# Kernel tuning notes

Measured on AMD Instinct MI355X. Metric: run time of the kernel, lower is better.

The kernel has to match this reference:

```python
import jax, jax.numpy as jnp
import numpy as np
import math

E = 16          # num_experts
TOP_K = 2       # num_experts_per_tok (used as capacity_factor in EC routing)
D = 1024        # embed_dim
F = 4096        # expert_hidden_dim = mlp_ratio * D
SH = 2048       # shared intermediate = F * n_shared_experts // mlp_ratio


def setup_inputs() -> dict:
    key = jax.random.key(0)
    ks = jax.random.split(key, 10)
    s = lambda k, shape, fan: jax.random.normal(k, shape, jnp.float32) / np.sqrt(fan)
    return {
        "x": jax.random.normal(ks[0], (32, 256, D), jnp.float32),
        "gate_w": s(ks[1], (E, D), D),                 # ECMoEGate.weight
        "up_w": s(ks[2], (E, F, D), D),                # fused_up.weight
        "up_b": s(ks[3], (E, F), D),                   # fused_up.bias
        "gw": s(ks[4], (E, F, D), D),                  # fused_gate.weight
        "gb": s(ks[5], (E, F), D),                     # fused_gate.bias
        "down_w": s(ks[6], (E, D, F), F),              # fused_down.weight
        "down_b": s(ks[7], (E, D), F),                 # fused_down.bias
        "sh_gate_w": s(ks[8], (SH, D), D),             # shared_experts.gate_proj
        "sh_up_w": s(ks[9], (SH, D), D),               # shared_experts.up_proj
        "sh_down_w": s(jax.random.fold_in(key, 11), (D, SH), SH),  # shared_experts.down_proj
    }


def reference(x, gate_w, up_w, up_b, gw, gb, down_w, down_b, sh_gate_w, sh_up_w, sh_down_w):
    B, S, Dm = x.shape
    h = x.reshape(-1, Dm)                               # [T, D]
    T = h.shape[0]
    # gate: sigmoid scores, expert-choice top-k over tokens per expert
    scores = jax.nn.sigmoid(h @ gate_w.T)               # [T, E]
    cap = math.ceil(T / E * TOP_K)                      # capacity per expert
    topk_score, topk_ids = jax.lax.top_k(scores.T, cap) # [E, cap]
    # dispatch: gather tokens per expert
    xin = h[topk_ids]                                   # [E, cap, D]
    # batched expert GLU (baddbmm equivalent)
    up = jnp.einsum('ecd,efd->ecf', xin, up_w) + up_b[:, None, :]
    g = jnp.einsum('ecd,efd->ecf', xin, gw) + gb[:, None, :]
    eo = jax.nn.silu(g) * up                            # [E, cap, F]
    eo = jnp.einsum('ecf,edf->ecd', eo, down_w) + down_b[:, None, :]
    # combine: weighted scatter-add back to token positions
    flat = (eo * topk_score[..., None]).reshape(-1, Dm) # [E*cap, D]
    out = jnp.zeros_like(h).at[topk_ids.reshape(-1)].add(flat)
    out = out.reshape(B, S, Dm)
    # shared dense GLU MLP (SiLU)
    shared = (jax.nn.silu(jnp.einsum('bsd,fd->bsf', x, sh_gate_w))
              * jnp.einsum('bsd,fd->bsf', x, sh_up_w))
    shared = jnp.einsum('bsf,df->bsd', shared, sh_down_w)
    return out + shared
```

## Files before the change

kernel.cpp:

```cpp
#include <hip/hip_runtime.h>
#include <hip/hip_bf16.h>

#define Tn 8192
#define Dn 1024
#define Fn 4096
#define SHn 2048
#define En 16
#define CAPn 1024

typedef __bf16 bf16_t;
typedef bf16_t bf16x8 __attribute__((ext_vector_type(8)));
typedef float f32x4 __attribute__((ext_vector_type(4)));

__device__ __forceinline__ unsigned short f2bf(float f) {
  unsigned int u = __builtin_bit_cast(unsigned int, f);
  u += 0x7FFFu + ((u >> 16) & 1u);
  return (unsigned short)(u >> 16);
}
__device__ __forceinline__ unsigned int pack2(float a, float b) {
  return (unsigned int)f2bf(a) | ((unsigned int)f2bf(b) << 16);
}

__device__ __forceinline__ void gload16(const void* g, void* l) {
  __builtin_amdgcn_global_load_lds(
      (const __attribute__((address_space(1))) unsigned int*)g,
      (__attribute__((address_space(3))) unsigned int*)l, 16, 0, 0);
}

__global__ __launch_bounds__(256) void kcvt(const float* __restrict__ s,
                                            unsigned short* __restrict__ d, int n8) {
  int i = blockIdx.x * 256 + threadIdx.x;
  int stride = gridDim.x * 256;
  const float4* sv = (const float4*)s;
  for (; i < n8; i += stride) {
    float4 a = sv[2 * i], b = sv[2 * i + 1];
    uint4 u = { pack2(a.x, a.y), pack2(a.z, a.w), pack2(b.x, b.y), pack2(b.z, b.w) };
    ((uint4*)d)[i] = u;
  }
}

__global__ __launch_bounds__(256) void kscores(const float* __restrict__ x,
                                               const float* __restrict__ gw,
                                               float* __restrict__ sc) {
  __shared__ float sx[Dn];
  int tid = threadIdx.x, tok = blockIdx.x;
  ((float4*)sx)[tid] = ((const float4*)(x + (size_t)tok * Dn))[tid];
  __syncthreads();
  int e = tid >> 4, kl = tid & 15;
  const float4* w = (const float4*)(gw + e * Dn);
  const float4* xv = (const float4*)sx;
  float acc = 0.f;
#pragma unroll
  for (int j = 0; j < 16; ++j) {
    float4 a = w[kl + 16 * j], b = xv[kl + 16 * j];
    acc += a.x * b.x + a.y * b.y + a.z * b.z + a.w * b.w;
  }
#pragma unroll
  for (int off = 8; off; off >>= 1) acc += __shfl_xor(acc, off, 64);
  if (kl == 0) sc[(size_t)e * Tn + tok] = 1.f / (1.f + expf(-acc));
}

__global__ __launch_bounds__(256) void kselect(const float* __restrict__ scores,
                                               int* __restrict__ ids,
                                               float* __restrict__ oscore) {
  __shared__ unsigned int keys[Tn];
  __shared__ unsigned int hist[256];
  __shared__ unsigned int sh_prefix, sh_k, sh_cnt, sh_eq;
  __shared__ int eqlist[1024];
  const int tid = threadIdx.x, e = blockIdx.x;
  const float* row = scores + (size_t)e * Tn;
  for (int i = 0; i < Tn / 256; ++i)
    keys[tid + i * 256] = __float_as_uint(row[tid + i * 256]);
  if (tid == 0) { sh_prefix = 0u; sh_k = CAPn; }
  __syncthreads();
  for (int shift = 24; shift >= 0; shift -= 8) {
    hist[tid] = 0u;
    __syncthreads();
    unsigned int prefix = sh_prefix;
    unsigned int mask = (shift == 24) ? 0u : (0xFFFFFFFFu << (shift + 8));
    for (int i = 0; i < Tn / 256; ++i) {
      unsigned int kk = keys[tid + i * 256];
      if ((kk & mask) == prefix) atomicAdd(&hist[(kk >> shift) & 255], 1u);
    }
    __syncthreads();
    if (tid == 0) {
      unsigned int k = sh_k, c = 0; int b;
      for (b = 255; b >= 0; --b) { c += hist[b]; if (c >= k) break; }
      sh_k = k - (c - hist[b]);
      sh_prefix = prefix | ((unsigned int)b << shift);
    }
    __syncthreads();
  }
  const unsigned int thr = sh_prefix;
  if (tid == 0) { sh_cnt = 0u; sh_eq = 0u; }
  __syncthreads();
  const int base = e * CAPn;
  for (int i = 0; i < Tn / 256; ++i) {
    int t = tid + i * 256;
    unsigned int kk = keys[t];
    if (kk > thr) {
      unsigned int p = atomicAdd(&sh_cnt, 1u);
      ids[base + p] = t;
      oscore[base + p] = __uint_as_float(kk);
    } else if (kk == thr) {
      unsigned int p = atomicAdd(&sh_eq, 1u);
      if (p < 1024u) eqlist[p] = t;
    }
  }
  __syncthreads();
  if (tid == 0) {
    int need = CAPn - (int)sh_cnt;
    int m = (int)sh_eq; if (m > 1024) m = 1024;
    for (int j = 0; j < need; ++j) {
      int best = 1 << 30, bi = 0;
      for (int i2 = 0; i2 < m; ++i2)
        if (eqlist[i2] < best) { best = eqlist[i2]; bi = i2; }
      eqlist[bi] = 1 << 30;
      ids[base + (int)sh_cnt + j] = best;
      oscore[base + (int)sh_cnt + j] = __uint_as_float(thr);
    }
  }
}

template <int BN, int NOPS, bool GATHER, int EPI>
__global__ __launch_bounds__(512, 2) void kgemm8(
    const unsigned short* __restrict__ Ab, const int* __restrict__ idsg,
    const unsigned short* __restrict__ B1b, const unsigned short* __restrict__ B2b,
    const float* __restrict__ bias1, const float* __restrict__ bias2,
    const float* __restrict__ scg, void* __restrict__ OutV,
    int N, int Mz, int K, int MBc, int NBc) {
  constexpr int BM = 256;
  constexpr int NF = (BN / 4) / 16;
  constexpr int BRPW = BN / 8;
  constexpr int BISS = BRPW / 8;
  constexpr unsigned A_OFF = 0;
  constexpr unsigned B1_OFF = 32768;
  constexpr unsigned B2_OFF = 32768u + (unsigned)BN * 128u;

  __shared__ alignas(16) unsigned char lds[2][65536];
  __shared__ int sIds[BM];
  __shared__ float sSc[BM];

  const int tid = threadIdx.x;
  const int lane = tid & 63, w = tid >> 6;
  const int wm = w >> 2, wn = w & 3;
  const int lrow = lane & 15, lk = lane >> 4;
  const int lr = lane >> 3, lc = lane & 7;
  const int srcb = ((lc ^ lr) << 4);

  const int nwg = gridDim.x;
  const int cpx = nwg >> 3;
  const int bid = blockIdx.x;
  const int swz = (bid & 7) * cpx + (bid >> 3);
  const int bm = swz % MBc;
  const int bn = (swz / MBc) % NBc;
  const int z  = swz / (NBc * MBc);
  const int row0 = bm * BM;

  if (tid < BM) {
    if (GATHER || EPI == 2) {
      sIds[tid] = idsg[z * CAPn + row0 + tid];
      if (EPI == 2) sSc[tid] = scg[z * CAPn + row0 + tid];
    }
  }
  __syncthreads();

  const size_t ks = (size_t)K * 2;
  const unsigned char* Az = (const unsigned char*)Ab + (EPI == 2 ? (size_t)z * Mz * ks : 0);
  const unsigned char* B1z = (const unsigned char*)B1b + (size_t)z * N * ks;
  const unsigned char* B2z = (NOPS == 2) ? (const unsigned char*)B2b + (size_t)z * N * ks : nullptr;

  const unsigned char* aS[4];
#pragma unroll
  for (int i = 0; i < 4; ++i) {
    int rr = w * 32 + 8 * i + lr;
    size_t arow = GATHER ? (size_t)sIds[rr] : (size_t)(row0 + rr);
    aS[i] = Az + arow * ks + srcb;
  }
  const unsigned char* b1S[BISS];
  const unsigned char* b2S[BISS];
#pragma unroll
  for (int i = 0; i < BISS; ++i) {
    int rr = bn * BN + w * BRPW + 8 * i + lr;
    b1S[i] = B1z + (size_t)rr * ks + srcb;
    if (NOPS == 2) b2S[i] = B2z + (size_t)rr * ks + srcb;
  }

  auto STG = [&](int idx, unsigned char* buf, int kb) {
    if (idx < 4) {
      gload16(aS[idx] + kb, buf + A_OFF + (unsigned)(w * 32 + 8 * idx) * 128u);
    } else if (NOPS == 2) {
      if (idx < 6)
        gload16(b1S[idx - 4] + kb, buf + B1_OFF + (unsigned)(w * BRPW + 8 * (idx - 4)) * 128u);
      else
        gload16(b2S[idx - 6] + kb, buf + B2_OFF + (unsigned)(w * BRPW + 8 * (idx - 6)) * 128u);
    } else {
      gload16(b1S[idx - 4] + kb, buf + B1_OFF + (unsigned)(w * BRPW + 8 * (idx - 4)) * 128u);
    }
  };

  f32x4 acc[NOPS][8][NF];
#pragma unroll
  for (int o = 0; o < NOPS; ++o)
#pragma unroll
    for (int m = 0; m < 8; ++m)
#pragma unroll
      for (int n = 0; n < NF; ++n) acc[o][m][n] = {0.f, 0.f, 0.f, 0.f};

#pragma unroll
  for (int i = 0; i < 8; ++i) STG(i, lds[0], 0);

  const int NT = K >> 6;
  int c = 0;
  for (int t = 0; t < NT; ++t) {
    unsigned char* bufc = lds[c];
    unsigned char* bufn = lds[c ^ 1];
    if (t + 1 < NT) {
      const int kb = (t + 1) * 128;
#pragma unroll
      for (int i = 0; i < 8; ++i) STG(i, bufn, kb);
      asm volatile("s_waitcnt vmcnt(8)" ::: "memory");
    } else {
      asm volatile("s_waitcnt vmcnt(0)" ::: "memory");
    }
    __builtin_amdgcn_s_barrier();
    __builtin_amdgcn_sched_barrier(0);

    bf16x8 bv[NOPS][NF][2];
#pragma unroll
    for (int n = 0; n < NF; ++n)
#pragma unroll
      for (int kk = 0; kk < 2; ++kk) {
        unsigned off = (unsigned)(wn * (BN / 4) + n * 16 + lrow) * 128u +
                       ((unsigned)((kk * 4 + lk) ^ (lrow & 7)) << 4);
        bv[0][n][kk] = *(const bf16x8*)(bufc + B1_OFF + off);
        if (NOPS == 2) bv[1][n][kk] = *(const bf16x8*)(bufc + B2_OFF + off);
      }
#pragma unroll
    for (int p = 0; p < 4; ++p) {
      bf16x8 av[2][2];
#pragma unroll
      for (int mm = 0; mm < 2; ++mm)
#pragma unroll
        for (int kk = 0; kk < 2; ++kk) {
          unsigned off = (unsigned)(wm * 128 + p * 32 + mm * 16 + lrow) * 128u +
                         ((unsigned)((kk * 4 + lk) ^ (lrow & 7)) << 4);
          av[mm][kk] = *(const bf16x8*)(bufc + A_OFF + off);
        }
      __builtin_amdgcn_s_setprio(1);
#pragma unroll
      for (int mm = 0; mm < 2; ++mm)
#pragma unroll
        for (int n = 0; n < NF; ++n)
#pragma unroll
          for (int kk = 0; kk < 2; ++kk) {
            acc[0][2 * p + mm][n] = __builtin_amdgcn_mfma_f32_16x16x32_bf16(
                av[mm][kk], bv[0][n][kk], acc[0][2 * p + mm][n], 0, 0, 0);
            if (NOPS == 2)
              acc[1][2 * p + mm][n] = __builtin_amdgcn_mfma_f32_16x16x32_bf16(
                  av[mm][kk], bv[1][n][kk], acc[1][2 * p + mm][n], 0, 0, 0);
          }
      __builtin_amdgcn_s_setprio(0);
    }
    __builtin_amdgcn_sched_barrier(0);
    __builtin_amdgcn_s_barrier();
    c ^= 1;
  }

  if (EPI == 0) {
    unsigned short* H = (unsigned short*)OutV;
#pragma unroll
    for (int n = 0; n < NF; ++n) {
      int col = bn * BN + wn * (BN / 4) + n * 16 + lrow;
      float bg = bias1 ? bias1[(size_t)z * N + col] : 0.f;
      float bu = bias2 ? bias2[(size_t)z * N + col] : 0.f;
#pragma unroll
      for (int mq = 0; mq < 8; ++mq) {
#pragma unroll
        for (int j = 0; j < 4; ++j) {
          float g = acc[0][mq][n][j] + bg;
          float u = (NOPS == 2 ? acc[1][mq][n][j] : 0.f) + bu;
          float h = g / (1.f + __expf(-g)) * u;
          int row = row0 + wm * 128 + mq * 16 + lk * 4 + j;
          H[(size_t)z * Mz * N + (size_t)row * N + col] = f2bf(h);
        }
      }
    }
  } else {
    float* Out = (float*)OutV;
#pragma unroll
    for (int n = 0; n < NF; ++n) {
      int col = bn * BN + wn * (BN / 4) + n * 16 + lrow;
      float bb = bias1 ? bias1[(size_t)z * N + col] : 0.f;
#pragma unroll
      for (int mq = 0; mq < 8; ++mq) {
#pragma unroll
        for (int j = 0; j < 4; ++j) {
          int rl = wm * 128 + mq * 16 + lk * 4 + j;
          float v = acc[0][mq][n][j] + bb;
          if (EPI == 2) {
            atomicAdd(Out + (size_t)sIds[rl] * Dn + col, sSc[rl] * v);
          } else {
            Out[(size_t)(row0 + rl) * Dn + col] = v;
          }
        }
      }
    }
  }
}

extern "C" void kernel_launch(void* const* d_in, const int* in_sizes, int n_in,
                              void* d_out, int out_size, void* d_ws, size_t ws_size,
                              hipStream_t stream) {
  const float* x      = (const float*)d_in[0];
  const float* gate_w = (const float*)d_in[1];
  const float* up_w   = (const float*)d_in[2];
  const float* up_b   = (const float*)d_in[3];
  const float* gw     = (const float*)d_in[4];
  const float* gb     = (const float*)d_in[5];
  const float* down_w = (const float*)d_in[6];
  const float* down_b = (const float*)d_in[7];
  const float* shg    = (const float*)d_in[8];
  const float* shu    = (const float*)d_in[9];
  const float* shd    = (const float*)d_in[10];
  float* out = (float*)d_out;

  const size_t H_BYTES  = (size_t)En * CAPn * Fn * 2;
  const size_t XB_BYTES = (size_t)Tn * Dn * 2;
  const size_t WE_BYTES = (size_t)En * Fn * Dn * 2;
  const size_t SH_BYTES = (size_t)SHn * Dn * 2;
  const size_t SC_BYTES = (size_t)En * Tn * 4;
  const size_t ID_BYTES = (size_t)En * CAPn * 4;
  const size_t need = H_BYTES + XB_BYTES + 3 * WE_BYTES + 3 * SH_BYTES +
                      SC_BYTES + 2 * ID_BYTES;
  if (ws_size < need) return;

  char* p = (char*)d_ws;
  unsigned short* H    = (unsigned short*)p; p += H_BYTES;
  unsigned short* xb   = (unsigned short*)p; p += XB_BYTES;
  unsigned short* upb  = (unsigned short*)p; p += WE_BYTES;
  unsigned short* gwb  = (unsigned short*)p; p += WE_BYTES;
  unsigned short* dwb  = (unsigned short*)p; p += WE_BYTES;
  unsigned short* shgb = (unsigned short*)p; p += SH_BYTES;
  unsigned short* shub = (unsigned short*)p; p += SH_BYTES;
  unsigned short* shdb = (unsigned short*)p; p += SH_BYTES;
  float* scores = (float*)p; p += SC_BYTES;
  int* ids      = (int*)p;  p += ID_BYTES;
  float* osc    = (float*)p;

  kcvt<<<2048, 256, 0, stream>>>(x, xb, Tn * Dn / 8);
  kscores<<<Tn, 256, 0, stream>>>(x, gate_w, scores);
  kselect<<<En, 256, 0, stream>>>(scores, ids, osc);
  kcvt<<<2048, 256, 0, stream>>>(up_w, upb, En * Fn * Dn / 8);
  kcvt<<<2048, 256, 0, stream>>>(gw, gwb, En * Fn * Dn / 8);
  kcvt<<<2048, 256, 0, stream>>>(down_w, dwb, En * Dn * Fn / 8);
  kcvt<<<256, 256, 0, stream>>>(shg, shgb, SHn * Dn / 8);
  kcvt<<<256, 256, 0, stream>>>(shu, shub, SHn * Dn / 8);
  kcvt<<<256, 256, 0, stream>>>(shd, shdb, Dn * SHn / 8);

  kgemm8<128, 2, false, 0><<<(Tn / 256) * (SHn / 128), 512, 0, stream>>>(
      xb, nullptr, shgb, shub, nullptr, nullptr, nullptr, H,
      SHn, Tn, Dn, Tn / 256, SHn / 128);
  kgemm8<256, 1, false, 1><<<(Tn / 256) * (Dn / 256), 512, 0, stream>>>(
      H, nullptr, shdb, nullptr, nullptr, nullptr, nullptr, out,
      Dn, Tn, SHn, Tn / 256, Dn / 256);
  kgemm8<128, 2, true, 0><<<(CAPn / 256) * (Fn / 128) * En, 512, 0, stream>>>(
      xb, ids, gwb, upb, gb, up_b, nullptr, H,
      Fn, CAPn, Dn, CAPn / 256, Fn / 128);
  kgemm8<256, 1, false, 2><<<(CAPn / 256) * (Dn / 256) * En, 512, 0, stream>>>(
      H, ids, dwb, nullptr, down_b, nullptr, osc, out,
      Dn, CAPn, Fn, CAPn / 256, Dn / 256);
}
```

Baseline: 994.2 us.

## Interleave next-tile global loads across MFMA phases and shrink shared-down tile

The GEMM main loop now spreads next-tile global-to-LDS loads across the four MFMA sub-phases instead of issuing them all up front, with barriers and lgkmcnt waits per phase. Load issue counts are generalized via NISS so BN=256 and single-operand variants issue the right number of loads. The shared down-projection GEMM switches from BN=256 to BN=128 tiles, doubling its grid. The extra per-phase barriers add synchronization overhead, and the waitcnt of 2 assumes a particular load ordering.

```diff
diff --git a/kernel.cpp b/kernel.cpp
--- a/kernel.cpp
+++ b/kernel.cpp
@@ -133,6 +133,7 @@
   constexpr int NF = (BN / 4) / 16;
   constexpr int BRPW = BN / 8;
   constexpr int BISS = BRPW / 8;
+  constexpr int NISS = 4 + BISS * NOPS;
   constexpr unsigned A_OFF = 0;
   constexpr unsigned B1_OFF = 32768;
   constexpr unsigned B2_OFF = 32768u + (unsigned)BN * 128u;
@@ -190,10 +191,10 @@
     if (idx < 4) {
       gload16(aS[idx] + kb, buf + A_OFF + (unsigned)(w * 32 + 8 * idx) * 128u);
     } else if (NOPS == 2) {
-      if (idx < 6)
+      if (idx < 4 + BISS)
         gload16(b1S[idx - 4] + kb, buf + B1_OFF + (unsigned)(w * BRPW + 8 * (idx - 4)) * 128u);
       else
-        gload16(b2S[idx - 6] + kb, buf + B2_OFF + (unsigned)(w * BRPW + 8 * (idx - 6)) * 128u);
+        gload16(b2S[idx - 4 - BISS] + kb, buf + B2_OFF + (unsigned)(w * BRPW + 8 * (idx - 4 - BISS)) * 128u);
     } else {
       gload16(b1S[idx - 4] + kb, buf + B1_OFF + (unsigned)(w * BRPW + 8 * (idx - 4)) * 128u);
     }
@@ -208,36 +209,38 @@
       for (int n = 0; n < NF; ++n) acc[o][m][n] = {0.f, 0.f, 0.f, 0.f};
 
 #pragma unroll
-  for (int i = 0; i < 8; ++i) STG(i, lds[0], 0);
+  for (int i = 0; i < NISS; ++i) STG(i, lds[0], 0);
 
   const int NT = K >> 6;
   int c = 0;
   for (int t = 0; t < NT; ++t) {
     unsigned char* bufc = lds[c];
     unsigned char* bufn = lds[c ^ 1];
-    if (t + 1 < NT) {
-      const int kb = (t + 1) * 128;
-#pragma unroll
-      for (int i = 0; i < 8; ++i) STG(i, bufn, kb);
-      asm volatile("s_waitcnt vmcnt(8)" ::: "memory");
-    } else {
-      asm volatile("s_waitcnt vmcnt(0)" ::: "memory");
-    }
-    __builtin_amdgcn_s_barrier();
-    __builtin_amdgcn_sched_barrier(0);
-
+    const bool pre = (t + 1 < NT);
+    const int kb = (t + 1) * 128;
     bf16x8 bv[NOPS][NF][2];
 #pragma unroll
-    for (int n = 0; n < NF; ++n)
-#pragma unroll
-      for (int kk = 0; kk < 2; ++kk) {
-        unsigned off = (unsigned)(wn * (BN / 4) + n * 16 + lrow) * 128u +
-                       ((unsigned)((kk * 4 + lk) ^ (lrow & 7)) << 4);
-        bv[0][n][kk] = *(const bf16x8*)(bufc + B1_OFF + off);
-        if (NOPS == 2) bv[1][n][kk] = *(const bf16x8*)(bufc + B2_OFF + off);
-      }
-#pragma unroll
     for (int p = 0; p < 4; ++p) {
+      if (pre) {
+        if (2 * p < NISS) STG(2 * p, bufn, kb);
+        if (2 * p + 1 < NISS) STG(2 * p + 1, bufn, kb);
+      }
+      if (p == 0) {
+        if (pre) asm volatile("s_waitcnt vmcnt(2)" ::: "memory");
+        else     asm volatile("s_waitcnt vmcnt(0)" ::: "memory");
+        __builtin_amdgcn_s_barrier();
+        __builtin_amdgcn_sched_barrier(0);
+#pragma unroll
+        for (int o = 0; o < NOPS; ++o)
+#pragma unroll
+          for (int n = 0; n < NF; ++n)
+#pragma unroll
+            for (int kk = 0; kk < 2; ++kk) {
+              unsigned off = (unsigned)(wn * (BN / 4) + n * 16 + lrow) * 128u +
+                             ((unsigned)((kk * 4 + lk) ^ (lrow & 7)) << 4);
+              bv[o][n][kk] = *(const bf16x8*)(bufc + (o ? B2_OFF : B1_OFF) + off);
+            }
+      }
       bf16x8 av[2][2];
 #pragma unroll
       for (int mm = 0; mm < 2; ++mm)
@@ -247,6 +250,12 @@
                          ((unsigned)((kk * 4 + lk) ^ (lrow & 7)) << 4);
           av[mm][kk] = *(const bf16x8*)(bufc + A_OFF + off);
         }
+      if (p != 0) {
+        __builtin_amdgcn_sched_barrier(0);
+        __builtin_amdgcn_s_barrier();
+      }
+      asm volatile("s_waitcnt lgkmcnt(0)" ::: "memory");
+      __builtin_amdgcn_sched_barrier(0);
       __builtin_amdgcn_s_setprio(1);
 #pragma unroll
       for (int mm = 0; mm < 2; ++mm)
@@ -261,9 +270,9 @@
                   av[mm][kk], bv[1][n][kk], acc[1][2 * p + mm][n], 0, 0, 0);
           }
       __builtin_amdgcn_s_setprio(0);
-    }
-    __builtin_amdgcn_sched_barrier(0);
-    __builtin_amdgcn_s_barrier();
+      __builtin_amdgcn_sched_barrier(0);
+      __builtin_amdgcn_s_barrier();
+    }
     c ^= 1;
   }
 
@@ -361,9 +370,9 @@
   kgemm8<128, 2, false, 0><<<(Tn / 256) * (SHn / 128), 512, 0, stream>>>(
       xb, nullptr, shgb, shub, nullptr, nullptr, nullptr, H,
       SHn, Tn, Dn, Tn / 256, SHn / 128);
-  kgemm8<256, 1, false, 1><<<(Tn / 256) * (Dn / 256), 512, 0, stream>>>(
+  kgemm8<128, 1, false, 1><<<(Tn / 256) * (Dn / 128), 512, 0, stream>>>(
       H, nullptr, shdb, nullptr, nullptr, nullptr, nullptr, out,
-      Dn, Tn, SHn, Tn / 256, Dn / 256);
+      Dn, Tn, SHn, Tn / 256, Dn / 128);
   kgemm8<128, 2, true, 0><<<(CAPn / 256) * (Fn / 128) * En, 512, 0, stream>>>(
       xb, ids, gwb, upb, gb, up_b, nullptr, H,
       Fn, CAPn, Dn, CAPn / 256, Fn / 128);
```

Result: slower. 1.214 ms (+22.1%).

## Split GEMM K-step into four quadrant phases interleaving staged loads with MFMA

Applied to the files above, without the earlier changes.

Replaces the GEMM kernel's single load-then-compute K iteration with four sub-phases. Each phase issues a partial global-to-LDS prefetch for the next tile, waits only on the loads it needs, and runs MFMAs on one 128x128 quadrant of the 256x256 (or 256x2x128) output tile. The LDS layout and the per-wave row mapping are reorganised to match. The aim is finer overlap of global memory traffic with matrix math and a smaller register footprint per phase, at the cost of more barriers per iteration and fiddlier vmcnt accounting.

```diff
diff --git a/kernel.cpp b/kernel.cpp
--- a/kernel.cpp
+++ b/kernel.cpp
@@ -122,28 +122,46 @@
   }
 }
 
-template <int BN, int NOPS, bool GATHER, int EPI>
-__global__ __launch_bounds__(512, 2) void kgemm8(
+#define READA(H)                                                              \
+  _Pragma("unroll") for (int mf = 0; mf < 4; ++mf)                            \
+  _Pragma("unroll") for (int kk = 0; kk < 2; ++kk)                            \
+    av[mf][kk] = *(const bf16x8*)(cur + (H) * 16384u +                        \
+        (unsigned)(wavem * 64 + mf * 16 + lrow) * 128u +                      \
+        ((unsigned)((kk * 4 + lk) ^ (lrow & 7)) << 4));
+
+#define READB(O)                                                              \
+  _Pragma("unroll") for (int nf = 0; nf < 2; ++nf)                            \
+  _Pragma("unroll") for (int kk = 0; kk < 2; ++kk)                            \
+    bv[O][nf][kk] = *(const bf16x8*)(cur + 32768u + (O) * 16384u +            \
+        (unsigned)(waven * 32 + nf * 16 + lrow) * 128u +                      \
+        ((unsigned)((kk * 4 + lk) ^ (lrow & 7)) << 4));
+
+#define MMACL(H, O)                                                           \
+  _Pragma("unroll") for (int mf = 0; mf < 4; ++mf)                            \
+  _Pragma("unroll") for (int nf = 0; nf < 2; ++nf)                            \
+  _Pragma("unroll") for (int kk = 0; kk < 2; ++kk)                            \
+    acc[H][O][mf][nf] = __builtin_amdgcn_mfma_f32_16x16x32_bf16(              \
+        av[mf][kk], bv[O][nf][kk], acc[H][O][mf][nf], 0, 0, 0);
+
+#define BARR __builtin_amdgcn_s_barrier()
+#define SCHED __builtin_amdgcn_sched_barrier(0)
+#define LGKM0 asm volatile("s_waitcnt lgkmcnt(0)" ::: "memory")
+
+template <int NOPS, bool GATHER, int EPI>
+__global__ __launch_bounds__(512, 2) void kgemm9(
     const unsigned short* __restrict__ Ab, const int* __restrict__ idsg,
     const unsigned short* __restrict__ B1b, const unsigned short* __restrict__ B2b,
     const float* __restrict__ bias1, const float* __restrict__ bias2,
     const float* __restrict__ scg, void* __restrict__ OutV,
     int N, int Mz, int K, int MBc, int NBc) {
   constexpr int BM = 256;
-  constexpr int NF = (BN / 4) / 16;
-  constexpr int BRPW = BN / 8;
-  constexpr int BISS = BRPW / 8;
-  constexpr unsigned A_OFF = 0;
-  constexpr unsigned B1_OFF = 32768;
-  constexpr unsigned B2_OFF = 32768u + (unsigned)BN * 128u;
-
   __shared__ alignas(16) unsigned char lds[2][65536];
   __shared__ int sIds[BM];
   __shared__ float sSc[BM];
 
   const int tid = threadIdx.x;
   const int lane = tid & 63, w = tid >> 6;
-  const int wm = w >> 2, wn = w & 3;
+  const int wavem = w >> 2, waven = w & 3;
   const int lrow = lane & 15, lk = lane >> 4;
   const int lr = lane >> 3, lc = lane & 7;
   const int srcb = ((lc ^ lr) << 4);
@@ -170,142 +188,142 @@
   const unsigned char* B1z = (const unsigned char*)B1b + (size_t)z * N * ks;
   const unsigned char* B2z = (NOPS == 2) ? (const unsigned char*)B2b + (size_t)z * N * ks : nullptr;
 
-  const unsigned char* aS[4];
+  const unsigned char* aR[4];
 #pragma unroll
   for (int i = 0; i < 4; ++i) {
-    int rr = w * 32 + 8 * i + lr;
+    int rr = i * 64 + w * 8 + lr;
     size_t arow = GATHER ? (size_t)sIds[rr] : (size_t)(row0 + rr);
-    aS[i] = Az + arow * ks + srcb;
-  }
-  const unsigned char* b1S[BISS];
-  const unsigned char* b2S[BISS];
-#pragma unroll
-  for (int i = 0; i < BISS; ++i) {
-    int rr = bn * BN + w * BRPW + 8 * i + lr;
-    b1S[i] = B1z + (size_t)rr * ks + srcb;
-    if (NOPS == 2) b2S[i] = B2z + (size_t)rr * ks + srcb;
-  }
-
-  auto STG = [&](int idx, unsigned char* buf, int kb) {
-    if (idx < 4) {
-      gload16(aS[idx] + kb, buf + A_OFF + (unsigned)(w * 32 + 8 * idx) * 128u);
-    } else if (NOPS == 2) {
-      if (idx < 6)
-        gload16(b1S[idx - 4] + kb, buf + B1_OFF + (unsigned)(w * BRPW + 8 * (idx - 4)) * 128u);
-      else
-        gload16(b2S[idx - 6] + kb, buf + B2_OFF + (unsigned)(w * BRPW + 8 * (idx - 6)) * 128u);
-    } else {
-      gload16(b1S[idx - 4] + kb, buf + B1_OFF + (unsigned)(w * BRPW + 8 * (idx - 4)) * 128u);
-    }
+    aR[i] = Az + arow * ks + srcb;
+  }
+  const unsigned char* bR[2][2];
+#pragma unroll
+  for (int o = 0; o < 2; ++o)
+#pragma unroll
+    for (int j = 0; j < 2; ++j) {
+      if (NOPS == 2) {
+        int rr = bn * 128 + j * 64 + w * 8 + lr;
+        bR[o][j] = (o ? B2z : B1z) + (size_t)rr * ks + srcb;
+      } else {
+        int rr = bn * 256 + o * 128 + j * 64 + w * 8 + lr;
+        bR[o][j] = B1z + (size_t)rr * ks + srcb;
+      }
+    }
+
+  auto stgA = [&](int i, unsigned char* buf, int kb) {
+    gload16(aR[i] + kb, buf + (unsigned)(i >> 1) * 16384u + (unsigned)(i & 1) * 8192u + (unsigned)w * 1024u);
   };
-
-  f32x4 acc[NOPS][8][NF];
-#pragma unroll
-  for (int o = 0; o < NOPS; ++o)
-#pragma unroll
-    for (int m = 0; m < 8; ++m)
-#pragma unroll
-      for (int n = 0; n < NF; ++n) acc[o][m][n] = {0.f, 0.f, 0.f, 0.f};
-
-#pragma unroll
-  for (int i = 0; i < 8; ++i) STG(i, lds[0], 0);
+  auto stgB = [&](int o, int j, unsigned char* buf, int kb) {
+    gload16(bR[o][j] + kb, buf + 32768u + (unsigned)o * 16384u + (unsigned)j * 8192u + (unsigned)w * 1024u);
+  };
+
+  f32x4 acc[2][2][4][2];
+#pragma unroll
+  for (int h = 0; h < 2; ++h)
+#pragma unroll
+    for (int o = 0; o < 2; ++o)
+#pragma unroll
+      for (int mf = 0; mf < 4; ++mf)
+#pragma unroll
+        for (int nf = 0; nf < 2; ++nf) acc[h][o][mf][nf] = {0.f, 0.f, 0.f, 0.f};
+
+  bf16x8 av[4][2], bv[2][2][2];
+
+  stgA(0, lds[0], 0); stgA(1, lds[0], 0);
+  stgB(0, 0, lds[0], 0); stgB(0, 1, lds[0], 0);
+  stgB(1, 0, lds[0], 0); stgB(1, 1, lds[0], 0);
+  stgA(2, lds[0], 0); stgA(3, lds[0], 0);
 
   const int NT = K >> 6;
-  int c = 0;
   for (int t = 0; t < NT; ++t) {
-    unsigned char* bufc = lds[c];
-    unsigned char* bufn = lds[c ^ 1];
-    if (t + 1 < NT) {
-      const int kb = (t + 1) * 128;
-#pragma unroll
-      for (int i = 0; i < 8; ++i) STG(i, bufn, kb);
-      asm volatile("s_waitcnt vmcnt(8)" ::: "memory");
-    } else {
-      asm volatile("s_waitcnt vmcnt(0)" ::: "memory");
-    }
-    __builtin_amdgcn_s_barrier();
-    __builtin_amdgcn_sched_barrier(0);
-
-    bf16x8 bv[NOPS][NF][2];
-#pragma unroll
-    for (int n = 0; n < NF; ++n)
-#pragma unroll
-      for (int kk = 0; kk < 2; ++kk) {
-        unsigned off = (unsigned)(wn * (BN / 4) + n * 16 + lrow) * 128u +
-                       ((unsigned)((kk * 4 + lk) ^ (lrow & 7)) << 4);
-        bv[0][n][kk] = *(const bf16x8*)(bufc + B1_OFF + off);
-        if (NOPS == 2) bv[1][n][kk] = *(const bf16x8*)(bufc + B2_OFF + off);
-      }
-#pragma unroll
-    for (int p = 0; p < 4; ++p) {
-      bf16x8 av[2][2];
-#pragma unroll
-      for (int mm = 0; mm < 2; ++mm)
-#pragma unroll
-        for (int kk = 0; kk < 2; ++kk) {
-          unsigned off = (unsigned)(wm * 128 + p * 32 + mm * 16 + lrow) * 128u +
-                         ((unsigned)((kk * 4 + lk) ^ (lrow & 7)) << 4);
-          av[mm][kk] = *(const bf16x8*)(bufc + A_OFF + off);
-        }
-      __builtin_amdgcn_s_setprio(1);
-#pragma unroll
-      for (int mm = 0; mm < 2; ++mm)
-#pragma unroll
-        for (int n = 0; n < NF; ++n)
-#pragma unroll
-          for (int kk = 0; kk < 2; ++kk) {
-            acc[0][2 * p + mm][n] = __builtin_amdgcn_mfma_f32_16x16x32_bf16(
-                av[mm][kk], bv[0][n][kk], acc[0][2 * p + mm][n], 0, 0, 0);
-            if (NOPS == 2)
-              acc[1][2 * p + mm][n] = __builtin_amdgcn_mfma_f32_16x16x32_bf16(
-                  av[mm][kk], bv[1][n][kk], acc[1][2 * p + mm][n], 0, 0, 0);
-          }
-      __builtin_amdgcn_s_setprio(0);
-    }
-    __builtin_amdgcn_sched_barrier(0);
-    __builtin_amdgcn_s_barrier();
-    c ^= 1;
+    unsigned char* cur = &lds[t & 1][0];
+    unsigned char* nxt = &lds[(t + 1) & 1][0];
+    const bool pre = (t + 1 < NT);
+    const int kb = (t + 1) * 128;
+
+    if (pre) { stgA(0, nxt, kb); stgA(1, nxt, kb); }
+    if (pre) asm volatile("s_waitcnt vmcnt(6)" ::: "memory");
+    else     asm volatile("s_waitcnt vmcnt(4)" ::: "memory");
+    BARR;
+    READA(0); READB(0);
+    LGKM0; SCHED;
+    __builtin_amdgcn_s_setprio(1);
+    MMACL(0, 0);
+    __builtin_amdgcn_s_setprio(0);
+    SCHED; BARR;
+
+    if (pre) { stgB(0, 0, nxt, kb); stgB(0, 1, nxt, kb); }
+    if (pre) asm volatile("s_waitcnt vmcnt(6)" ::: "memory");
+    else     asm volatile("s_waitcnt vmcnt(2)" ::: "memory");
+    BARR;
+    READB(1);
+    LGKM0; SCHED;
+    __builtin_amdgcn_s_setprio(1);
+    MMACL(0, 1);
+    __builtin_amdgcn_s_setprio(0);
+    SCHED; BARR;
+
+    if (pre) { stgB(1, 0, nxt, kb); stgB(1, 1, nxt, kb); }
+    if (pre) asm volatile("s_waitcnt vmcnt(6)" ::: "memory");
+    else     asm volatile("s_waitcnt vmcnt(0)" ::: "memory");
+    BARR;
+    READA(1);
+    LGKM0; SCHED;
+    __builtin_amdgcn_s_setprio(1);
+    MMACL(1, 1);
+    __builtin_amdgcn_s_setprio(0);
+    SCHED; BARR;
+
+    if (pre) { stgA(2, nxt, kb); stgA(3, nxt, kb); }
+    BARR;
+    __builtin_amdgcn_s_setprio(1);
+    MMACL(1, 0);
+    __builtin_amdgcn_s_setprio(0);
+    SCHED; BARR;
   }
 
   if (EPI == 0) {
     unsigned short* H = (unsigned short*)OutV;
 #pragma unroll
-    for (int n = 0; n < NF; ++n) {
-      int col = bn * BN + wn * (BN / 4) + n * 16 + lrow;
+    for (int nf = 0; nf < 2; ++nf) {
+      int col = bn * 128 + waven * 32 + nf * 16 + lrow;
       float bg = bias1 ? bias1[(size_t)z * N + col] : 0.f;
       float bu = bias2 ? bias2[(size_t)z * N + col] : 0.f;
 #pragma unroll
-      for (int mq = 0; mq < 8; ++mq) {
-#pragma unroll
-        for (int j = 0; j < 4; ++j) {
-          float g = acc[0][mq][n][j] + bg;
-          float u = (NOPS == 2 ? acc[1][mq][n][j] : 0.f) + bu;
-          float h = g / (1.f + __expf(-g)) * u;
-          int row = row0 + wm * 128 + mq * 16 + lk * 4 + j;
-          H[(size_t)z * Mz * N + (size_t)row * N + col] = f2bf(h);
-        }
-      }
+      for (int h = 0; h < 2; ++h)
+#pragma unroll
+        for (int mf = 0; mf < 4; ++mf)
+#pragma unroll
+          for (int j = 0; j < 4; ++j) {
+            float g = acc[h][0][mf][nf][j] + bg;
+            float u = acc[h][1][mf][nf][j] + bu;
+            float hv = g / (1.f + __expf(-g)) * u;
+            int row = row0 + h * 128 + wavem * 64 + mf * 16 + lk * 4 + j;
+            H[(size_t)z * Mz * N + (size_t)row * N + col] = f2bf(hv);
+          }
     }
   } else {
     float* Out = (float*)OutV;
 #pragma unroll
-    for (int n = 0; n < NF; ++n) {
-      int col = bn * BN + wn * (BN / 4) + n * 16 + lrow;
-      float bb = bias1 ? bias1[(size_t)z * N + col] : 0.f;
-#pragma unroll
-      for (int mq = 0; mq < 8; ++mq) {
-#pragma unroll
-        for (int j = 0; j < 4; ++j) {
-          int rl = wm * 128 + mq * 16 + lk * 4 + j;
-          float v = acc[0][mq][n][j] + bb;
-          if (EPI == 2) {
-            atomicAdd(Out + (size_t)sIds[rl] * Dn + col, sSc[rl] * v);
-          } else {
-            Out[(size_t)(row0 + rl) * Dn + col] = v;
-          }
-        }
+    for (int o = 0; o < 2; ++o)
+#pragma unroll
+      for (int nf = 0; nf < 2; ++nf) {
+        int col = bn * 256 + o * 128 + waven * 32 + nf * 16 + lrow;
+        float bb = bias1 ? bias1[(size_t)z * N + col] : 0.f;
+#pragma unroll
+        for (int h = 0; h < 2; ++h)
+#pragma unroll
+          for (int mf = 0; mf < 4; ++mf)
+#pragma unroll
+            for (int j = 0; j < 4; ++j) {
+              int rl = h * 128 + wavem * 64 + mf * 16 + lk * 4 + j;
+              float v = acc[h][o][mf][nf][j] + bb;
+              if (EPI == 2) {
+                atomicAdd(Out + (size_t)sIds[rl] * Dn + col, sSc[rl] * v);
+              } else {
+                Out[(size_t)(row0 + rl) * Dn + col] = v;
+              }
+            }
       }
-    }
   }
 }
 
@@ -358,16 +376,16 @@
   kcvt<<<256, 256, 0, stream>>>(shu, shub, SHn * Dn / 8);
   kcvt<<<256, 256, 0, stream>>>(shd, shdb, Dn * SHn / 8);
 
-  kgemm8<128, 2, false, 0><<<(Tn / 256) * (SHn / 128), 512, 0, stream>>>(
+  kgemm9<2, false, 0><<<(Tn / 256) * (SHn / 128), 512, 0, stream>>>(
       xb, nullptr, shgb, shub, nullptr, nullptr, nullptr, H,
       SHn, Tn, Dn, Tn / 256, SHn / 128);
-  kgemm8<256, 1, false, 1><<<(Tn / 256) * (Dn / 256), 512, 0, stream>>>(
+  kgemm9<1, false, 1><<<(Tn / 256) * (Dn / 256), 512, 0, stream>>>(
       H, nullptr, shdb, nullptr, nullptr, nullptr, nullptr, out,
       Dn, Tn, SHn, Tn / 256, Dn / 256);
-  kgemm8<128, 2, true, 0><<<(CAPn / 256) * (Fn / 128) * En, 512, 0, stream>>>(
+  kgemm9<2, true, 0><<<(CAPn / 256) * (Fn / 128) * En, 512, 0, stream>>>(
       xb, ids, gwb, upb, gb, up_b, nullptr, H,
       Fn, CAPn, Dn, CAPn / 256, Fn / 128);
-  kgemm8<256, 1, false, 2><<<(CAPn / 256) * (Dn / 256) * En, 512, 0, stream>>>(
+  kgemm9<1, false, 2><<<(CAPn / 256) * (Dn / 256) * En, 512, 0, stream>>>(
       H, ids, dwb, nullptr, down_b, nullptr, osc, out,
       Dn, CAPn, Fn, CAPn / 256, Dn / 256);
 }
```

New measurement: 1.136 ms. 1.14x slower.

## Replace 256x256 double-buffered GEMMs with 128x128 single-buffered 32x32 MFMA kernels

Applied to the files above, without the earlier changes.

Replaces the templated 512-thread, 256-row-tile, double-buffered GEMM with two specialized 256-thread kernels. These use 128x128 tiles, single-buffered LDS staging and the 32x32x16 bf16 MFMA. Smaller tiles give more workgroups and higher occupancy, and the larger MFMA shape cuts LDS read traffic per flop. In exchange it drops the prefetch pipelining, which exposes global load latency at each k-step behind two barriers, and it lowers per-tile data reuse.

```diff
diff --git a/kernel.cpp b/kernel.cpp
--- a/kernel.cpp
+++ b/kernel.cpp
@@ -11,6 +11,7 @@
 typedef __bf16 bf16_t;
 typedef bf16_t bf16x8 __attribute__((ext_vector_type(8)));
 typedef float f32x4 __attribute__((ext_vector_type(4)));
+typedef float f32x16 __attribute__((ext_vector_type(16)));
 
 __device__ __forceinline__ unsigned short f2bf(float f) {
   unsigned int u = __builtin_bit_cast(unsigned int, f);
@@ -122,187 +123,194 @@
   }
 }
 
-template <int BN, int NOPS, bool GATHER, int EPI>
-__global__ __launch_bounds__(512, 2) void kgemm8(
-    const unsigned short* __restrict__ Ab, const int* __restrict__ idsg,
-    const unsigned short* __restrict__ B1b, const unsigned short* __restrict__ B2b,
-    const float* __restrict__ bias1, const float* __restrict__ bias2,
-    const float* __restrict__ scg, void* __restrict__ OutV,
-    int N, int Mz, int K, int MBc, int NBc) {
-  constexpr int BM = 256;
-  constexpr int NF = (BN / 4) / 16;
-  constexpr int BRPW = BN / 8;
-  constexpr int BISS = BRPW / 8;
-  constexpr unsigned A_OFF = 0;
-  constexpr unsigned B1_OFF = 32768;
-  constexpr unsigned B2_OFF = 32768u + (unsigned)BN * 128u;
-
-  __shared__ alignas(16) unsigned char lds[2][65536];
-  __shared__ int sIds[BM];
-  __shared__ float sSc[BM];
-
+
+template <bool GATHER>
+__global__ __launch_bounds__(256, 2) void kglu_bf(
+    const unsigned short* __restrict__ X, const int* __restrict__ idsg,
+    const unsigned short* __restrict__ Wg, const unsigned short* __restrict__ Wu,
+    const float* __restrict__ biasg, const float* __restrict__ biasu,
+    unsigned short* __restrict__ H, int N, int Mz, int MB, int NB) {
+  constexpr int K = Dn;
+  __shared__ alignas(16) unsigned char sA[16384];
+  __shared__ alignas(16) unsigned char sB1[16384];
+  __shared__ alignas(16) unsigned char sB2[16384];
+  __shared__ int sIds[128];
   const int tid = threadIdx.x;
-  const int lane = tid & 63, w = tid >> 6;
-  const int wm = w >> 2, wn = w & 3;
-  const int lrow = lane & 15, lk = lane >> 4;
-  const int lr = lane >> 3, lc = lane & 7;
-  const int srcb = ((lc ^ lr) << 4);
-
   const int nwg = gridDim.x;
   const int cpx = nwg >> 3;
   const int bid = blockIdx.x;
   const int swz = (bid & 7) * cpx + (bid >> 3);
-  const int bm = swz % MBc;
-  const int bn = (swz / MBc) % NBc;
-  const int z  = swz / (NBc * MBc);
-  const int row0 = bm * BM;
-
-  if (tid < BM) {
-    if (GATHER || EPI == 2) {
-      sIds[tid] = idsg[z * CAPn + row0 + tid];
-      if (EPI == 2) sSc[tid] = scg[z * CAPn + row0 + tid];
-    }
-  }
-  __syncthreads();
-
-  const size_t ks = (size_t)K * 2;
-  const unsigned char* Az = (const unsigned char*)Ab + (EPI == 2 ? (size_t)z * Mz * ks : 0);
-  const unsigned char* B1z = (const unsigned char*)B1b + (size_t)z * N * ks;
-  const unsigned char* B2z = (NOPS == 2) ? (const unsigned char*)B2b + (size_t)z * N * ks : nullptr;
-
-  const unsigned char* aS[4];
+  const int bm = swz % MB;
+  const int bn = (swz / MB) % NB;
+  const int z  = swz / (MB * NB);
+  const int lane = tid & 63, w = tid >> 6;
+  const int wm = w >> 1, wn = w & 1;
+  const int row32 = lane & 31, kh = lane >> 5;
+  const int row0 = bm * 128;
+
+  if (tid < 128) sIds[tid] = GATHER ? idsg[z * CAPn + row0 + tid] : (row0 + tid);
+  __syncthreads();
+
+  const int lr = lane >> 3;
+  const int lc = lane & 7;
+  const int srcb = ((lc ^ lr) << 4);
+  const unsigned char* Xb = (const unsigned char*)X;
+  const unsigned char* Gb = (const unsigned char*)Wg + (size_t)z * N * (K * 2);
+  const unsigned char* Ub = (const unsigned char*)Wu + (size_t)z * N * (K * 2);
+  const unsigned char* aP[4];
 #pragma unroll
   for (int i = 0; i < 4; ++i) {
-    int rr = w * 32 + 8 * i + lr;
-    size_t arow = GATHER ? (size_t)sIds[rr] : (size_t)(row0 + rr);
-    aS[i] = Az + arow * ks + srcb;
-  }
-  const unsigned char* b1S[BISS];
-  const unsigned char* b2S[BISS];
-#pragma unroll
-  for (int i = 0; i < BISS; ++i) {
-    int rr = bn * BN + w * BRPW + 8 * i + lr;
-    b1S[i] = B1z + (size_t)rr * ks + srcb;
-    if (NOPS == 2) b2S[i] = B2z + (size_t)rr * ks + srcb;
-  }
-
-  auto STG = [&](int idx, unsigned char* buf, int kb) {
-    if (idx < 4) {
-      gload16(aS[idx] + kb, buf + A_OFF + (unsigned)(w * 32 + 8 * idx) * 128u);
-    } else if (NOPS == 2) {
-      if (idx < 6)
-        gload16(b1S[idx - 4] + kb, buf + B1_OFF + (unsigned)(w * BRPW + 8 * (idx - 4)) * 128u);
-      else
-        gload16(b2S[idx - 6] + kb, buf + B2_OFF + (unsigned)(w * BRPW + 8 * (idx - 6)) * 128u);
-    } else {
-      gload16(b1S[idx - 4] + kb, buf + B1_OFF + (unsigned)(w * BRPW + 8 * (idx - 4)) * 128u);
-    }
-  };
-
-  f32x4 acc[NOPS][8][NF];
-#pragma unroll
-  for (int o = 0; o < NOPS; ++o)
-#pragma unroll
-    for (int m = 0; m < 8; ++m)
-#pragma unroll
-      for (int n = 0; n < NF; ++n) acc[o][m][n] = {0.f, 0.f, 0.f, 0.f};
-
-#pragma unroll
-  for (int i = 0; i < 8; ++i) STG(i, lds[0], 0);
-
-  const int NT = K >> 6;
-  int c = 0;
-  for (int t = 0; t < NT; ++t) {
-    unsigned char* bufc = lds[c];
-    unsigned char* bufn = lds[c ^ 1];
-    if (t + 1 < NT) {
-      const int kb = (t + 1) * 128;
-#pragma unroll
-      for (int i = 0; i < 8; ++i) STG(i, bufn, kb);
-      asm volatile("s_waitcnt vmcnt(8)" ::: "memory");
-    } else {
-      asm volatile("s_waitcnt vmcnt(0)" ::: "memory");
-    }
-    __builtin_amdgcn_s_barrier();
-    __builtin_amdgcn_sched_barrier(0);
-
-    bf16x8 bv[NOPS][NF][2];
-#pragma unroll
-    for (int n = 0; n < NF; ++n)
-#pragma unroll
-      for (int kk = 0; kk < 2; ++kk) {
-        unsigned off = (unsigned)(wn * (BN / 4) + n * 16 + lrow) * 128u +
-                       ((unsigned)((kk * 4 + lk) ^ (lrow & 7)) << 4);
-        bv[0][n][kk] = *(const bf16x8*)(bufc + B1_OFF + off);
-        if (NOPS == 2) bv[1][n][kk] = *(const bf16x8*)(bufc + B2_OFF + off);
+    int ar = w * 32 + 8 * i + lr;
+    aP[i] = Xb + (size_t)sIds[ar] * (K * 2) + srcb;
+  }
+  const int br0 = bn * 128 + w * 32 + lr;
+  const unsigned char* gP0 = Gb + (size_t)br0 * (K * 2) + srcb;
+  const unsigned char* uP0 = Ub + (size_t)br0 * (K * 2) + srcb;
+
+  f32x16 accG[2][2], accU[2][2];
+#pragma unroll
+  for (int m = 0; m < 2; ++m)
+#pragma unroll
+    for (int n = 0; n < 2; ++n) {
+      accG[m][n] = (f32x16)(0.f);
+      accU[m][n] = (f32x16)(0.f);
+    }
+
+  for (int k0b = 0; k0b < K * 2; k0b += 128) {
+    __syncthreads();
+#pragma unroll
+    for (int i = 0; i < 4; ++i) {
+      unsigned ldsoff = (unsigned)(w * 32 + 8 * i) * 128u;
+      gload16(aP[i] + k0b, sA + ldsoff);
+      gload16(gP0 + (size_t)i * 8 * (K * 2) + k0b, sB1 + ldsoff);
+      gload16(uP0 + (size_t)i * 8 * (K * 2) + k0b, sB2 + ldsoff);
+    }
+    __syncthreads();
+#pragma unroll
+    for (int ks = 0; ks < 4; ++ks) {
+      const int swb = (((ks * 2 + kh) ^ (row32 & 7)) << 4);
+      bf16x8 av[2], gv[2], uv[2];
+#pragma unroll
+      for (int m = 0; m < 2; ++m)
+        av[m] = *(const bf16x8*)(sA + (wm * 64 + m * 32 + row32) * 128 + swb);
+#pragma unroll
+      for (int n = 0; n < 2; ++n) {
+        gv[n] = *(const bf16x8*)(sB1 + (wn * 64 + n * 32 + row32) * 128 + swb);
+        uv[n] = *(const bf16x8*)(sB2 + (wn * 64 + n * 32 + row32) * 128 + swb);
       }
 #pragma unroll
-    for (int p = 0; p < 4; ++p) {
-      bf16x8 av[2][2];
-#pragma unroll
-      for (int mm = 0; mm < 2; ++mm)
-#pragma unroll
-        for (int kk = 0; kk < 2; ++kk) {
-          unsigned off = (unsigned)(wm * 128 + p * 32 + mm * 16 + lrow) * 128u +
-                         ((unsigned)((kk * 4 + lk) ^ (lrow & 7)) << 4);
-          av[mm][kk] = *(const bf16x8*)(bufc + A_OFF + off);
+      for (int m = 0; m < 2; ++m)
+#pragma unroll
+        for (int n = 0; n < 2; ++n) {
+          accG[m][n] = __builtin_amdgcn_mfma_f32_32x32x16_bf16(av[m], gv[n], accG[m][n], 0, 0, 0);
+          accU[m][n] = __builtin_amdgcn_mfma_f32_32x32x16_bf16(av[m], uv[n], accU[m][n], 0, 0, 0);
         }
-      __builtin_amdgcn_s_setprio(1);
-#pragma unroll
-      for (int mm = 0; mm < 2; ++mm)
-#pragma unroll
-        for (int n = 0; n < NF; ++n)
-#pragma unroll
-          for (int kk = 0; kk < 2; ++kk) {
-            acc[0][2 * p + mm][n] = __builtin_amdgcn_mfma_f32_16x16x32_bf16(
-                av[mm][kk], bv[0][n][kk], acc[0][2 * p + mm][n], 0, 0, 0);
-            if (NOPS == 2)
-              acc[1][2 * p + mm][n] = __builtin_amdgcn_mfma_f32_16x16x32_bf16(
-                  av[mm][kk], bv[1][n][kk], acc[1][2 * p + mm][n], 0, 0, 0);
-          }
-      __builtin_amdgcn_s_setprio(0);
-    }
-    __builtin_amdgcn_sched_barrier(0);
-    __builtin_amdgcn_s_barrier();
-    c ^= 1;
-  }
-
-  if (EPI == 0) {
-    unsigned short* H = (unsigned short*)OutV;
-#pragma unroll
-    for (int n = 0; n < NF; ++n) {
-      int col = bn * BN + wn * (BN / 4) + n * 16 + lrow;
-      float bg = bias1 ? bias1[(size_t)z * N + col] : 0.f;
-      float bu = bias2 ? bias2[(size_t)z * N + col] : 0.f;
-#pragma unroll
-      for (int mq = 0; mq < 8; ++mq) {
-#pragma unroll
-        for (int j = 0; j < 4; ++j) {
-          float g = acc[0][mq][n][j] + bg;
-          float u = (NOPS == 2 ? acc[1][mq][n][j] : 0.f) + bu;
-          float h = g / (1.f + __expf(-g)) * u;
-          int row = row0 + wm * 128 + mq * 16 + lk * 4 + j;
-          H[(size_t)z * Mz * N + (size_t)row * N + col] = f2bf(h);
-        }
+    }
+  }
+#pragma unroll
+  for (int n = 0; n < 2; ++n) {
+    int col = bn * 128 + wn * 64 + n * 32 + row32;
+    float bg = biasg ? biasg[(size_t)z * N + col] : 0.f;
+    float bu = biasu ? biasu[(size_t)z * N + col] : 0.f;
+#pragma unroll
+    for (int m = 0; m < 2; ++m) {
+#pragma unroll
+      for (int reg = 0; reg < 16; ++reg) {
+        float g = accG[m][n][reg] + bg;
+        float u = accU[m][n][reg] + bu;
+        float h = g / (1.f + __expf(-g)) * u;
+        int row = row0 + wm * 64 + m * 32 + (reg & 3) + 8 * (reg >> 2) + 4 * kh;
+        H[(size_t)z * Mz * N + (size_t)row * N + col] = f2bf(h);
       }
     }
-  } else {
-    float* Out = (float*)OutV;
-#pragma unroll
-    for (int n = 0; n < NF; ++n) {
-      int col = bn * BN + wn * (BN / 4) + n * 16 + lrow;
-      float bb = bias1 ? bias1[(size_t)z * N + col] : 0.f;
-#pragma unroll
-      for (int mq = 0; mq < 8; ++mq) {
-#pragma unroll
-        for (int j = 0; j < 4; ++j) {
-          int rl = wm * 128 + mq * 16 + lk * 4 + j;
-          float v = acc[0][mq][n][j] + bb;
-          if (EPI == 2) {
-            atomicAdd(Out + (size_t)sIds[rl] * Dn + col, sSc[rl] * v);
-          } else {
-            Out[(size_t)(row0 + rl) * Dn + col] = v;
-          }
+  }
+}
+
+template <int K, bool SCATTER>
+__global__ __launch_bounds__(256, 2) void kdown_bf(
+    const unsigned short* __restrict__ Hin, const unsigned short* __restrict__ W,
+    const float* __restrict__ bias, const int* __restrict__ idsg,
+    const float* __restrict__ scg, float* __restrict__ Out, int Mz, int MB, int NB) {
+  constexpr int N = Dn;
+  __shared__ alignas(16) unsigned char sA[16384];
+  __shared__ alignas(16) unsigned char sB[16384];
+  __shared__ int sIds[128];
+  __shared__ float sSc[128];
+  const int tid = threadIdx.x;
+  const int nwg = gridDim.x;
+  const int cpx = nwg >> 3;
+  const int bid = blockIdx.x;
+  const int swz = (bid & 7) * cpx + (bid >> 3);
+  const int bm = swz % MB;
+  const int bn = (swz / MB) % NB;
+  const int z  = swz / (MB * NB);
+  const int lane = tid & 63, w = tid >> 6;
+  const int wm = w >> 1, wn = w & 1;
+  const int row32 = lane & 31, kh = lane >> 5;
+  const int row0 = bm * 128;
+
+  if (SCATTER && tid < 128) {
+    sIds[tid] = idsg[z * CAPn + row0 + tid];
+    sSc[tid] = scg[z * CAPn + row0 + tid];
+  }
+  __syncthreads();
+
+  const int lr = lane >> 3;
+  const int lc = lane & 7;
+  const int srcb = ((lc ^ lr) << 4);
+  const unsigned char* Ab = (const unsigned char*)Hin + (size_t)z * Mz * (K * 2);
+  const unsigned char* Wb = (const unsigned char*)W + (size_t)z * N * (K * 2);
+  const int ar0 = row0 + w * 32 + lr;
+  const int br0 = bn * 128 + w * 32 + lr;
+  const unsigned char* aP0 = Ab + (size_t)ar0 * (K * 2) + srcb;
+  const unsigned char* bP0 = Wb + (size_t)br0 * (K * 2) + srcb;
+
+  f32x16 acc[2][2];
+#pragma unroll
+  for (int m = 0; m < 2; ++m)
+#pragma unroll
+    for (int n = 0; n < 2; ++n) acc[m][n] = (f32x16)(0.f);
+
+  for (int k0b = 0; k0b < K * 2; k0b += 128) {
+    __syncthreads();
+#pragma unroll
+    for (int i = 0; i < 4; ++i) {
+      unsigned ldsoff = (unsigned)(w * 32 + 8 * i) * 128u;
+      gload16(aP0 + (size_t)i * 8 * (K * 2) + k0b, sA + ldsoff);
+      gload16(bP0 + (size_t)i * 8 * (K * 2) + k0b, sB + ldsoff);
+    }
+    __syncthreads();
+#pragma unroll
+    for (int ks = 0; ks < 4; ++ks) {
+      const int swb = (((ks * 2 + kh) ^ (row32 & 7)) << 4);
+      bf16x8 av[2], bv[2];
+#pragma unroll
+      for (int m = 0; m < 2; ++m)
+        av[m] = *(const bf16x8*)(sA + (wm * 64 + m * 32 + row32) * 128 + swb);
+#pragma unroll
+      for (int n = 0; n < 2; ++n)
+        bv[n] = *(const bf16x8*)(sB + (wn * 64 + n * 32 + row32) * 128 + swb);
+#pragma unroll
+      for (int m = 0; m < 2; ++m)
+#pragma unroll
+        for (int n = 0; n < 2; ++n)
+          acc[m][n] = __builtin_amdgcn_mfma_f32_32x32x16_bf16(av[m], bv[n], acc[m][n], 0, 0, 0);
+    }
+  }
+#pragma unroll
+  for (int n = 0; n < 2; ++n) {
+    int col = bn * 128 + wn * 64 + n * 32 + row32;
+    float bvv = bias ? bias[(size_t)z * N + col] : 0.f;
+#pragma unroll
+    for (int m = 0; m < 2; ++m) {
+#pragma unroll
+      for (int reg = 0; reg < 16; ++reg) {
+        int rl = wm * 64 + m * 32 + (reg & 3) + 8 * (reg >> 2) + 4 * kh;
+        float v = acc[m][n][reg] + bvv;
+        if (SCATTER) {
+          atomicAdd(Out + (size_t)sIds[rl] * Dn + col, sSc[rl] * v);
+        } else {
+          Out[(size_t)(row0 + rl) * Dn + col] = v;
         }
       }
     }
@@ -358,16 +366,13 @@
   kcvt<<<256, 256, 0, stream>>>(shu, shub, SHn * Dn / 8);
   kcvt<<<256, 256, 0, stream>>>(shd, shdb, Dn * SHn / 8);
 
-  kgemm8<128, 2, false, 0><<<(Tn / 256) * (SHn / 128), 512, 0, stream>>>(
-      xb, nullptr, shgb, shub, nullptr, nullptr, nullptr, H,
-      SHn, Tn, Dn, Tn / 256, SHn / 128);
-  kgemm8<256, 1, false, 1><<<(Tn / 256) * (Dn / 256), 512, 0, stream>>>(
-      H, nullptr, shdb, nullptr, nullptr, nullptr, nullptr, out,
-      Dn, Tn, SHn, Tn / 256, Dn / 256);
-  kgemm8<128, 2, true, 0><<<(CAPn / 256) * (Fn / 128) * En, 512, 0, stream>>>(
-      xb, ids, gwb, upb, gb, up_b, nullptr, H,
-      Fn, CAPn, Dn, CAPn / 256, Fn / 128);
-  kgemm8<256, 1, false, 2><<<(CAPn / 256) * (Dn / 256) * En, 512, 0, stream>>>(
-      H, ids, dwb, nullptr, down_b, nullptr, osc, out,
-      Dn, CAPn, Fn, CAPn / 256, Dn / 256);
-}
+  kglu_bf<false><<<(Tn / 128) * (SHn / 128), 256, 0, stream>>>(
+      xb, nullptr, shgb, shub, nullptr, nullptr, H, SHn, Tn, Tn / 128, SHn / 128);
+  kdown_bf<SHn, false><<<(Tn / 128) * (Dn / 128), 256, 0, stream>>>(
+      H, shdb, nullptr, nullptr, nullptr, out, Tn, Tn / 128, Dn / 128);
+
+  kglu_bf<true><<<(CAPn / 128) * (Fn / 128) * En, 256, 0, stream>>>(
+      xb, ids, gwb, upb, gb, up_b, H, Fn, CAPn, CAPn / 128, Fn / 128);
+  kdown_bf<Fn, true><<<(CAPn / 128) * (Dn / 128) * En, 256, 0, stream>>>(
+      H, dwb, down_b, ids, osc, out, CAPn, CAPn / 128, Dn / 128);
+}
```

Result: no change. 997.3 us (+0.3%).
